# Performance work log

Hardware: AMD Instinct MI355X
Metric: run time of the kernel (lower is better)

The kernel has to match this reference:

```python
import jax, jax.numpy as jnp
import numpy as np


def setup_inputs() -> dict:
    key = jax.random.key(0)
    k1, k2 = jax.random.split(key)
    support_features = jax.random.normal(k1, (1000, 5, 512), dtype=jnp.float32)
    query_features = jax.random.normal(k2, (5000, 512), dtype=jnp.float32)
    return {"support_features": support_features, "query_features": query_features, "use_cosine": 1}


def reference(support_features, query_features, use_cosine):
    # Preprocess: mean-center over (classes, shots), then L2-normalize per vector.
    mean = jnp.mean(support_features, axis=(0, 1), keepdims=True)  # [1,1,D]
    s = support_features - mean                                    # [C,S,D]
    q = query_features - mean[0]                                   # [Q,D]
    s = s / jnp.linalg.norm(s, axis=2, keepdims=True)
    q = q / jnp.linalg.norm(q, axis=1, keepdims=True)
    if use_cosine:
        # cosine sims without materializing [C,Q,S,D]; einsum fuses the dot.
        sims = jnp.einsum('csd,qd->cqs', s, q)   # [C,Q,S]
        best = jnp.max(sims, axis=2)             # [C,Q] best shot per class
        return jnp.argmax(best, axis=0)          # [Q] predicted class
    else:
        # euclidean cdist(query[Q,D], support[C,S,D]) -> [C,Q,S]
        d2 = (jnp.sum(q * q, axis=1)[None, :, None]
              + jnp.sum(s * s, axis=2)[:, None, :]
              - 2.0 * jnp.einsum('csd,qd->cqs', s, q))
        dist = jnp.sqrt(jnp.maximum(d2, 0.0))
        best = jnp.min(dist, axis=2)
        return jnp.argmin(best, axis=0)
```

## Files before the change

kernel.cpp:

```cpp
#include <hip/hip_runtime.h>
#include <stdint.h>

#define D     512
#define NSUP  5000
#define NQRY  5000
#define NPAD  5120
#define MEAN_BLOCKS 100
#define ROWS_PER_MEAN_BLOCK 50
#define SCALE 512.0f

#define OFF_SHI     0
#define OFF_SLO     5242880
#define OFF_QHI     10485760
#define OFF_QLO     15728640
#define OFF_PARTIAL 20971520
#define OFF_MEAN    21176320
#define OFF_KEYS    21178368

typedef _Float16 half4v __attribute__((ext_vector_type(4)));
typedef _Float16 half8v __attribute__((ext_vector_type(8)));
typedef float    f32x4  __attribute__((ext_vector_type(4)));

__device__ __forceinline__ unsigned long long pack_key(float v, int sidx) {
    unsigned u = __float_as_uint(v);
    u = (u & 0x80000000u) ? ~u : (u | 0x80000000u);
    return ((unsigned long long)u << 32) | (unsigned)(0xFFFFFFFFu - (unsigned)sidx);
}

__device__ __forceinline__ void gload16(const void* g, void* l) {
    __builtin_amdgcn_global_load_lds(
        (const __attribute__((address_space(1))) unsigned int*)g,
        (__attribute__((address_space(3))) unsigned int*)l, 16, 0, 0);
}

__global__ void k_partial_mean(const float* __restrict__ sup, float* __restrict__ partial) {
    const int col = threadIdx.x;
    const int b   = blockIdx.x;
    const int r0  = b * ROWS_PER_MEAN_BLOCK;
    float acc = 0.0f;
    #pragma unroll 5
    for (int r = 0; r < ROWS_PER_MEAN_BLOCK; ++r)
        acc += sup[(size_t)(r0 + r) * D + col];
    partial[b * D + col] = acc;
}

__global__ void k_mean_init(const float* __restrict__ partial, float* __restrict__ mean,
                            unsigned long long* __restrict__ keys) {
    const int col = threadIdx.x;
    float acc = 0.0f;
    #pragma unroll 4
    for (int b = 0; b < MEAN_BLOCKS; ++b) acc += partial[b * D + col];
    mean[col] = acc * (1.0f / (float)NSUP);
    for (int i = col; i < NSUP; i += 512) keys[i] = 0ull;
}

__global__ void k_split(const float* __restrict__ sup, const float* __restrict__ qry,
                        const float* __restrict__ mean,
                        _Float16* __restrict__ shi, _Float16* __restrict__ slo,
                        _Float16* __restrict__ qhi, _Float16* __restrict__ qlo) {
    const int t    = threadIdx.x;
    const int rloc = t >> 7;
    const int tc   = t & 127;
    const int b    = (int)blockIdx.x * 4 + rloc;
    const float* src; _Float16 *dhi, *dlo; int valid;
    if (b < NPAD) { src = sup + (size_t)b * D;
                    dhi = shi + (size_t)b * D; dlo = slo + (size_t)b * D; valid = (b < NSUP); }
    else          { int r = b - NPAD; src = qry + (size_t)r * D;
                    dhi = qhi + (size_t)r * D; dlo = qlo + (size_t)r * D; valid = (r < NQRY); }
    __shared__ float red[8];
    if (!valid) {
        half4v z = {};
        *(half4v*)(dhi + tc * 4) = z;
        *(half4v*)(dlo + tc * 4) = z;
        return;
    }
    float4 v = *(const float4*)(src + tc * 4);
    float4 m = *(const float4*)(mean + tc * 4);
    v.x -= m.x; v.y -= m.y; v.z -= m.z; v.w -= m.w;
    float ss = v.x * v.x + v.y * v.y + v.z * v.z + v.w * v.w;
    #pragma unroll
    for (int off = 32; off > 0; off >>= 1) ss += __shfl_down(ss, off, 64);
    if ((t & 63) == 0) red[t >> 6] = ss;
    __syncthreads();
    const float rn = SCALE / sqrtf(red[rloc * 2] + red[rloc * 2 + 1]);
    float sv[4] = {v.x * rn, v.y * rn, v.z * rn, v.w * rn};
    half4v h, l;
    #pragma unroll
    for (int i = 0; i < 4; ++i) {
        _Float16 hh = (_Float16)sv[i];
        h[i] = hh;
        l[i] = (_Float16)(sv[i] - (float)hh);
    }
    *(half4v*)(dhi + tc * 4) = h;
    *(half4v*)(dlo + tc * 4) = l;
}

__launch_bounds__(256)
__global__ void k_main(const _Float16* __restrict__ shi, const _Float16* __restrict__ slo,
                       const _Float16* __restrict__ qhi, const _Float16* __restrict__ qlo,
                       unsigned long long* __restrict__ keys) {
    __shared__ __align__(16) _Float16 lds_shi[2 * 4096];
    __shared__ __align__(16) _Float16 lds_slo[2 * 4096];
    __shared__ __align__(16) _Float16 lds_qhi[2 * 4096];
    __shared__ __align__(16) _Float16 lds_qlo[2 * 4096];
    __shared__ unsigned long long kl[128];

    const int tid  = threadIdx.x;
    const int lane = tid & 63;
    const int wv   = tid >> 6;
    const int q0   = blockIdx.x * 128;
    const int s0   = blockIdx.y * 128;

    const int m0  = wv * 32 + (lane >> 2);
    const int m1  = m0 + 16;
    const int sl0 = ((lane & 3) ^ ((m0 >> 1) & 3)) * 16;
    const int sl1 = ((lane & 3) ^ ((m1 >> 1) & 3)) * 16;
    const char* pShi = (const char*)shi; const char* pSlo = (const char*)slo;
    const char* pQhi = (const char*)qhi; const char* pQlo = (const char*)qlo;
    const size_t rS0 = (size_t)(s0 + m0) * 1024 + sl0;
    const size_t rS1 = (size_t)(s0 + m1) * 1024 + sl1;
    const size_t rQ0 = (size_t)(q0 + m0) * 1024 + sl0;
    const size_t rQ1 = (size_t)(q0 + m1) * 1024 + sl1;
    _Float16* d_shi0 = lds_shi + wv * 1024;      _Float16* d_shi1 = lds_shi + wv * 1024 + 512;
    _Float16* d_slo0 = lds_slo + wv * 1024;      _Float16* d_slo1 = lds_slo + wv * 1024 + 512;
    _Float16* d_qhi0 = lds_qhi + wv * 1024;      _Float16* d_qhi1 = lds_qhi + wv * 1024 + 512;
    _Float16* d_qlo0 = lds_qlo + wv * 1024;      _Float16* d_qlo1 = lds_qlo + wv * 1024 + 512;

    const int l15 = lane & 15;
    const int kg  = lane >> 4;
    const int fo  = l15 * 64 + ((kg ^ ((l15 >> 1) & 3)) * 16);
    const int sm  = (wv & 1) * 64;
    const int qm  = (wv >> 1) * 64;
    const char* fShi = (const char*)lds_shi + (size_t)sm * 64 + fo;
    const char* fSlo = (const char*)lds_slo + (size_t)sm * 64 + fo;
    const char* fQhi = (const char*)lds_qhi + (size_t)qm * 64 + fo;
    const char* fQlo = (const char*)lds_qlo + (size_t)qm * 64 + fo;

    f32x4 acc[4][4] = {};
    if (tid < 128) kl[tid] = 0ull;

#define STAGE(B, KC) do {                                                          \
        const size_t kb_ = (size_t)(KC) * 2;                                       \
        gload16(pShi + rS0 + kb_, d_shi0 + (B) * 4096);                            \
        gload16(pShi + rS1 + kb_, d_shi1 + (B) * 4096);                            \
        gload16(pSlo + rS0 + kb_, d_slo0 + (B) * 4096);                            \
        gload16(pSlo + rS1 + kb_, d_slo1 + (B) * 4096);                            \
        gload16(pQhi + rQ0 + kb_, d_qhi0 + (B) * 4096);                            \
        gload16(pQhi + rQ1 + kb_, d_qhi1 + (B) * 4096);                            \
        gload16(pQlo + rQ0 + kb_, d_qlo0 + (B) * 4096);                            \
        gload16(pQlo + rQ1 + kb_, d_qlo1 + (B) * 4096);                            \
    } while (0)

#define COMPUTE(B) do {                                                            \
        half8v ah[4], al[4], bh[4], bl[4];                                         \
        _Pragma("unroll")                                                          \
        for (int f = 0; f < 4; ++f) {                                              \
            ah[f] = *(const half8v*)(fShi + (B) * 8192 + f * 1024);                \
            al[f] = *(const half8v*)(fSlo + (B) * 8192 + f * 1024);                \
            bh[f] = *(const half8v*)(fQhi + (B) * 8192 + f * 1024);                \
            bl[f] = *(const half8v*)(fQlo + (B) * 8192 + f * 1024);                \
        }                                                                          \
        _Pragma("unroll")                                                          \
        for (int fa = 0; fa < 4; ++fa)                                             \
            _Pragma("unroll")                                                      \
            for (int fb = 0; fb < 4; ++fb) {                                       \
                acc[fa][fb] = __builtin_amdgcn_mfma_f32_16x16x32_f16(ah[fa], bh[fb], acc[fa][fb], 0, 0, 0); \
                acc[fa][fb] = __builtin_amdgcn_mfma_f32_16x16x32_f16(ah[fa], bl[fb], acc[fa][fb], 0, 0, 0); \
                acc[fa][fb] = __builtin_amdgcn_mfma_f32_16x16x32_f16(al[fa], bh[fb], acc[fa][fb], 0, 0, 0); \
            }                                                                      \
    } while (0)

    STAGE(0, 0);
    __syncthreads();

    for (int i = 0; i < 8; ++i) {
        const int kc = i * 64;
        STAGE(1, kc + 32);
        COMPUTE(0);
        __syncthreads();
        if (i < 7) STAGE(0, kc + 64);
        COMPUTE(1);
        __syncthreads();
    }
#undef STAGE
#undef COMPUTE

    #pragma unroll
    for (int fb = 0; fb < 4; ++fb) {
        unsigned long long best = 0ull;
        #pragma unroll
        for (int fa = 0; fa < 4; ++fa)
            #pragma unroll
            for (int r = 0; r < 4; ++r) {
                const int s = s0 + sm + fa * 16 + kg * 4 + r;
                if (s < NSUP) {
                    unsigned long long k = pack_key(acc[fa][fb][r], s);
                    if (k > best) best = k;
                }
            }
        unsigned long long o = __shfl_xor(best, 16, 64); if (o > best) best = o;
        o = __shfl_xor(best, 32, 64);                    if (o > best) best = o;
        if (kg == 0) atomicMax(&kl[qm + fb * 16 + l15], best);
    }
    __syncthreads();
    if (tid < 128) {
        const int q = q0 + tid;
        if (q < NQRY && kl[tid] != 0ull) atomicMax(&keys[q], kl[tid]);
    }
}

__global__ void k_decode(const unsigned long long* __restrict__ keys, int* __restrict__ out) {
    const int q = blockIdx.x * 256 + threadIdx.x;
    if (q < NQRY) {
        unsigned sidx = 0xFFFFFFFFu - (unsigned)(keys[q] & 0xFFFFFFFFull);
        out[q] = (int)(sidx / 5u);
    }
}

extern "C" void kernel_launch(void* const* d_in, const int* in_sizes, int n_in,
                              void* d_out, int out_size, void* d_ws, size_t ws_size,
                              hipStream_t stream) {
    const float* sup = (const float*)d_in[0];
    const float* qry = (const float*)d_in[1];
    int* out = (int*)d_out;

    char* ws = (char*)d_ws;
    _Float16* shi = (_Float16*)(ws + OFF_SHI);
    _Float16* slo = (_Float16*)(ws + OFF_SLO);
    _Float16* qhi = (_Float16*)(ws + OFF_QHI);
    _Float16* qlo = (_Float16*)(ws + OFF_QLO);
    float* partial = (float*)(ws + OFF_PARTIAL);
    float* mean    = (float*)(ws + OFF_MEAN);
    unsigned long long* keys = (unsigned long long*)(ws + OFF_KEYS);

    k_partial_mean<<<MEAN_BLOCKS, 512, 0, stream>>>(sup, partial);
    k_mean_init<<<1, 512, 0, stream>>>(partial, mean, keys);
    k_split<<<(2 * NPAD) / 4, 512, 0, stream>>>(sup, qry, mean, shi, slo, qhi, qlo);
    dim3 grid(NPAD / 128, NPAD / 128);
    k_main<<<grid, 256, 0, stream>>>(shi, slo, qhi, qlo, keys);
    k_decode<<<(NQRY + 255) / 256, 256, 0, stream>>>(keys, out);
}
```

Measured before the change: 184.1 us.

## Enlarge main GEMM tile to 256x256 with 8 waves and explicit pipelining

The similarity kernel moves from 128x128 tiles with 4 waves to 256x256 tiles with 8 waves, each wave computing 128x64 of the output. It stages 32-wide K slices into a double-buffered 130KB dynamic LDS region, using explicit vmcnt/lgkmcnt waits, raw s_barrier and setprio around the MFMA bursts. The larger tile raises arithmetic intensity and cuts global re-reads. In exchange there are far fewer blocks (400 on 256 CUs, so a poor wave quantization), heavy LDS use that limits blocks per CU despite the launch bound of 2, and higher register pressure from 32 accumulators.

```diff
diff --git a/kernel.cpp b/kernel.cpp
--- a/kernel.cpp
+++ b/kernel.cpp
@@ -16,6 +16,13 @@
 #define OFF_PARTIAL 20971520
 #define OFF_MEAN    21176320
 #define OFF_KEYS    21178368
+
+#define SH_SHI   0
+#define SH_SLO   32768
+#define SH_QHI   65536
+#define SH_QLO   98304
+#define SH_KL    131072
+#define SH_TOTAL (131072 + 2048)
 
 typedef _Float16 half4v __attribute__((ext_vector_type(4)));
 typedef _Float16 half8v __attribute__((ext_vector_type(8)));
@@ -95,104 +102,129 @@
     *(half4v*)(dlo + tc * 4) = l;
 }
 
-__launch_bounds__(256)
+__launch_bounds__(512, 2)
 __global__ void k_main(const _Float16* __restrict__ shi, const _Float16* __restrict__ slo,
                        const _Float16* __restrict__ qhi, const _Float16* __restrict__ qlo,
                        unsigned long long* __restrict__ keys) {
-    __shared__ __align__(16) _Float16 lds_shi[2 * 4096];
-    __shared__ __align__(16) _Float16 lds_slo[2 * 4096];
-    __shared__ __align__(16) _Float16 lds_qhi[2 * 4096];
-    __shared__ __align__(16) _Float16 lds_qlo[2 * 4096];
-    __shared__ unsigned long long kl[128];
+    extern __shared__ char smem[];
+    char* lshi = smem + SH_SHI;
+    char* lslo = smem + SH_SLO;
+    char* lqhi = smem + SH_QHI;
+    char* lqlo = smem + SH_QLO;
+    unsigned long long* kl = (unsigned long long*)(smem + SH_KL);
 
     const int tid  = threadIdx.x;
     const int lane = tid & 63;
     const int wv   = tid >> 6;
-    const int q0   = blockIdx.x * 128;
-    const int s0   = blockIdx.y * 128;
-
-    const int m0  = wv * 32 + (lane >> 2);
-    const int m1  = m0 + 16;
-    const int sl0 = ((lane & 3) ^ ((m0 >> 1) & 3)) * 16;
-    const int sl1 = ((lane & 3) ^ ((m1 >> 1) & 3)) * 16;
+    const int q0   = blockIdx.x * 256;
+    const int s0   = blockIdx.y * 256;
+    const int wr   = wv >> 2;
+    const int wc   = wv & 3;
+
+    if (tid < 256) kl[tid] = 0ull;
+
+    const int srow = wv * 16 + (lane >> 2);
+    const int sl0  = ((lane & 3) ^ ((lane >> 3) & 3)) * 16;
+    const size_t gA0 = (size_t)(s0 + srow) * 1024 + sl0;
+    const size_t gB0 = (size_t)(q0 + srow) * 1024 + sl0;
     const char* pShi = (const char*)shi; const char* pSlo = (const char*)slo;
     const char* pQhi = (const char*)qhi; const char* pQlo = (const char*)qlo;
-    const size_t rS0 = (size_t)(s0 + m0) * 1024 + sl0;
-    const size_t rS1 = (size_t)(s0 + m1) * 1024 + sl1;
-    const size_t rQ0 = (size_t)(q0 + m0) * 1024 + sl0;
-    const size_t rQ1 = (size_t)(q0 + m1) * 1024 + sl1;
-    _Float16* d_shi0 = lds_shi + wv * 1024;      _Float16* d_shi1 = lds_shi + wv * 1024 + 512;
-    _Float16* d_slo0 = lds_slo + wv * 1024;      _Float16* d_slo1 = lds_slo + wv * 1024 + 512;
-    _Float16* d_qhi0 = lds_qhi + wv * 1024;      _Float16* d_qhi1 = lds_qhi + wv * 1024 + 512;
-    _Float16* d_qlo0 = lds_qlo + wv * 1024;      _Float16* d_qlo1 = lds_qlo + wv * 1024 + 512;
+    const int dst0 = wv * 1024;
+    const int dst1 = 8192 + wv * 1024;
 
     const int l15 = lane & 15;
     const int kg  = lane >> 4;
-    const int fo  = l15 * 64 + ((kg ^ ((l15 >> 1) & 3)) * 16);
-    const int sm  = (wv & 1) * 64;
-    const int qm  = (wv >> 1) * 64;
-    const char* fShi = (const char*)lds_shi + (size_t)sm * 64 + fo;
-    const char* fSlo = (const char*)lds_slo + (size_t)sm * 64 + fo;
-    const char* fQhi = (const char*)lds_qhi + (size_t)qm * 64 + fo;
-    const char* fQlo = (const char*)lds_qlo + (size_t)qm * 64 + fo;
-
-    f32x4 acc[4][4] = {};
-    if (tid < 128) kl[tid] = 0ull;
-
-#define STAGE(B, KC) do {                                                          \
-        const size_t kb_ = (size_t)(KC) * 2;                                       \
-        gload16(pShi + rS0 + kb_, d_shi0 + (B) * 4096);                            \
-        gload16(pShi + rS1 + kb_, d_shi1 + (B) * 4096);                            \
-        gload16(pSlo + rS0 + kb_, d_slo0 + (B) * 4096);                            \
-        gload16(pSlo + rS1 + kb_, d_slo1 + (B) * 4096);                            \
-        gload16(pQhi + rQ0 + kb_, d_qhi0 + (B) * 4096);                            \
-        gload16(pQhi + rQ1 + kb_, d_qhi1 + (B) * 4096);                            \
-        gload16(pQlo + rQ0 + kb_, d_qlo0 + (B) * 4096);                            \
-        gload16(pQlo + rQ1 + kb_, d_qlo1 + (B) * 4096);                            \
-    } while (0)
-
-#define COMPUTE(B) do {                                                            \
-        half8v ah[4], al[4], bh[4], bl[4];                                         \
-        _Pragma("unroll")                                                          \
-        for (int f = 0; f < 4; ++f) {                                              \
-            ah[f] = *(const half8v*)(fShi + (B) * 8192 + f * 1024);                \
-            al[f] = *(const half8v*)(fSlo + (B) * 8192 + f * 1024);                \
-            bh[f] = *(const half8v*)(fQhi + (B) * 8192 + f * 1024);                \
-            bl[f] = *(const half8v*)(fQlo + (B) * 8192 + f * 1024);                \
-        }                                                                          \
-        _Pragma("unroll")                                                          \
-        for (int fa = 0; fa < 4; ++fa)                                             \
-            _Pragma("unroll")                                                      \
-            for (int fb = 0; fb < 4; ++fb) {                                       \
-                acc[fa][fb] = __builtin_amdgcn_mfma_f32_16x16x32_f16(ah[fa], bh[fb], acc[fa][fb], 0, 0, 0); \
-                acc[fa][fb] = __builtin_amdgcn_mfma_f32_16x16x32_f16(ah[fa], bl[fb], acc[fa][fb], 0, 0, 0); \
-                acc[fa][fb] = __builtin_amdgcn_mfma_f32_16x16x32_f16(al[fa], bh[fb], acc[fa][fb], 0, 0, 0); \
-            }                                                                      \
+    const int swz = (kg ^ ((l15 >> 1) & 3)) * 16;
+    const int foA = (wr * 128 + l15) * 64 + swz;
+    const int foB = (wc * 64  + l15) * 64 + swz;
+
+    f32x4 acc[8][4] = {};
+
+#define BAR()    asm volatile("s_barrier" ::: "memory")
+#define WAITV8() asm volatile("s_waitcnt vmcnt(8)" ::: "memory")
+#define WAITV0() asm volatile("s_waitcnt vmcnt(0)" ::: "memory")
+#define WAITL()  asm volatile("s_waitcnt lgkmcnt(0)" ::: "memory")
+
+#define STAGE(P, KT) do {                                                   \
+        const size_t kb_ = (size_t)(KT) * 64;                               \
+        gload16(pShi + gA0 + kb_,          lshi + (P) * 16384 + dst0);      \
+        gload16(pShi + gA0 + 131072 + kb_, lshi + (P) * 16384 + dst1);      \
+        gload16(pSlo + gA0 + kb_,          lslo + (P) * 16384 + dst0);      \
+        gload16(pSlo + gA0 + 131072 + kb_, lslo + (P) * 16384 + dst1);      \
+        gload16(pQhi + gB0 + kb_,          lqhi + (P) * 16384 + dst0);      \
+        gload16(pQhi + gB0 + 131072 + kb_, lqhi + (P) * 16384 + dst1);      \
+        gload16(pQlo + gB0 + kb_,          lqlo + (P) * 16384 + dst0);      \
+        gload16(pQlo + gB0 + 131072 + kb_, lqlo + (P) * 16384 + dst1);      \
+    } while (0)
+
+#define RD_A(P, QA) do { _Pragma("unroll")                                  \
+        for (int i_ = 0; i_ < 4; ++i_) {                                    \
+            ah[i_] = *(const half8v*)(lshi + (P)*16384 + foA + ((QA)*4 + i_)*1024); \
+            al[i_] = *(const half8v*)(lslo + (P)*16384 + foA + ((QA)*4 + i_)*1024); \
+        } } while (0)
+
+#define RD_B(P, QB) do { _Pragma("unroll")                                  \
+        for (int j_ = 0; j_ < 2; ++j_) {                                    \
+            bh[j_] = *(const half8v*)(lqhi + (P)*16384 + foB + ((QB)*2 + j_)*1024); \
+            bl[j_] = *(const half8v*)(lqlo + (P)*16384 + foB + ((QB)*2 + j_)*1024); \
+        } } while (0)
+
+#define MMA(QA, QB) do {                                                    \
+        __builtin_amdgcn_s_setprio(1);                                      \
+        _Pragma("unroll")                                                   \
+        for (int i_ = 0; i_ < 4; ++i_)                                      \
+        { _Pragma("unroll")                                                 \
+          for (int j_ = 0; j_ < 2; ++j_) {                                  \
+            f32x4* a_ = &acc[(QA)*4 + i_][(QB)*2 + j_];                     \
+            *a_ = __builtin_amdgcn_mfma_f32_16x16x32_f16(ah[i_], bh[j_], *a_, 0, 0, 0); \
+            *a_ = __builtin_amdgcn_mfma_f32_16x16x32_f16(ah[i_], bl[j_], *a_, 0, 0, 0); \
+            *a_ = __builtin_amdgcn_mfma_f32_16x16x32_f16(al[i_], bh[j_], *a_, 0, 0, 0); \
+          } }                                                               \
+        __builtin_amdgcn_s_setprio(0);                                      \
+        __builtin_amdgcn_sched_barrier(0);                                  \
+    } while (0)
+
+#define COMPUTE_TILE(P) do {                                                \
+        half8v ah[4], al[4], bh[2], bl[2];                                  \
+        RD_A(P, 0); RD_B(P, 0); MMA(0, 0);                                  \
+        RD_B(P, 1);             MMA(0, 1);                                  \
+        RD_A(P, 1); RD_B(P, 0); MMA(1, 0);                                  \
+        RD_B(P, 1);             MMA(1, 1);                                  \
+    } while (0)
+
+#define HALF(P, TT) do {                                                    \
+        COMPUTE_TILE(P);                                                    \
+        WAITL(); BAR();                       \
+        if ((TT) + 2 < 16) { STAGE(P, (TT) + 2); WAITV8(); }                \
+        else               { WAITV0(); }                                    \
+        BAR();                                \
     } while (0)
 
     STAGE(0, 0);
-    __syncthreads();
-
-    for (int i = 0; i < 8; ++i) {
-        const int kc = i * 64;
-        STAGE(1, kc + 32);
-        COMPUTE(0);
-        __syncthreads();
-        if (i < 7) STAGE(0, kc + 64);
-        COMPUTE(1);
-        __syncthreads();
-    }
+    STAGE(1, 1);
+    WAITV8();
+    BAR();
+
+    for (int t = 0; t < 16; t += 2) {
+        HALF(0, t);
+        HALF(1, t + 1);
+    }
+
+#undef HALF
+#undef COMPUTE_TILE
+#undef MMA
+#undef RD_B
+#undef RD_A
 #undef STAGE
-#undef COMPUTE
 
     #pragma unroll
     for (int fb = 0; fb < 4; ++fb) {
         unsigned long long best = 0ull;
         #pragma unroll
-        for (int fa = 0; fa < 4; ++fa)
+        for (int fa = 0; fa < 8; ++fa)
             #pragma unroll
             for (int r = 0; r < 4; ++r) {
-                const int s = s0 + sm + fa * 16 + kg * 4 + r;
+                const int s = s0 + wr * 128 + fa * 16 + kg * 4 + r;
                 if (s < NSUP) {
                     unsigned long long k = pack_key(acc[fa][fb][r], s);
                     if (k > best) best = k;
@@ -200,10 +232,10 @@
             }
         unsigned long long o = __shfl_xor(best, 16, 64); if (o > best) best = o;
         o = __shfl_xor(best, 32, 64);                    if (o > best) best = o;
-        if (kg == 0) atomicMax(&kl[qm + fb * 16 + l15], best);
+        if (kg == 0) atomicMax(&kl[wc * 64 + fb * 16 + l15], best);
     }
     __syncthreads();
-    if (tid < 128) {
+    if (tid < 256) {
         const int q = q0 + tid;
         if (q < NQRY && kl[tid] != 0ull) atomicMax(&keys[q], kl[tid]);
     }
@@ -233,10 +265,17 @@
     float* mean    = (float*)(ws + OFF_MEAN);
     unsigned long long* keys = (unsigned long long*)(ws + OFF_KEYS);
 
+    static bool attr_set = false;
+    if (!attr_set) {
+        (void)hipFuncSetAttribute((const void*)k_main,
+                                  hipFuncAttributeMaxDynamicSharedMemorySize, SH_TOTAL);
+        attr_set = true;
+    }
+
     k_partial_mean<<<MEAN_BLOCKS, 512, 0, stream>>>(sup, partial);
     k_mean_init<<<1, 512, 0, stream>>>(partial, mean, keys);
     k_split<<<(2 * NPAD) / 4, 512, 0, stream>>>(sup, qry, mean, shi, slo, qhi, qlo);
-    dim3 grid(NPAD / 128, NPAD / 128);
-    k_main<<<grid, 256, 0, stream>>>(shi, slo, qhi, qlo, keys);
+    dim3 grid(NPAD / 256, NPAD / 256);
+    k_main<<<grid, 512, SH_TOTAL, stream>>>(shi, slo, qhi, qlo, keys);
     k_decode<<<(NQRY + 255) / 256, 256, 0, stream>>>(keys, out);
 }
```

Measured after the change: 174.7 us. 1.05x faster.
